# Optimization experiments

Measured on AMD Instinct MI355X. Metric: run time of the kernel, lower is better.

The kernel has to match this reference:

```python
import jax, jax.numpy as jnp
import numpy as np

NEG = -1e30


def setup_inputs() -> dict:
    key = jax.random.key(0)
    ks = jax.random.split(key, 8)
    B, d, Lc, Lq = 32, 128, 2048, 512
    C = jax.random.normal(ks[0], (B, d, Lc), dtype=jnp.float32)
    Q = jax.random.normal(ks[1], (B, d, Lq), dtype=jnp.float32)
    Cmask = jax.random.randint(ks[2], (B, Lc), 0, 2, dtype=jnp.int32)
    Qmask = jax.random.randint(ks[3], (B, Lq), 0, 2, dtype=jnp.int32)
    # xavier_uniform over (d, 1): bound = sqrt(6 / (d + 1))
    bnd = float(np.sqrt(6.0 / (d + 1)))
    w_c = jax.random.uniform(ks[4], (d, 1), minval=-bnd, maxval=bnd, dtype=jnp.float32)
    w_q = jax.random.uniform(ks[5], (d, 1), minval=-bnd, maxval=bnd, dtype=jnp.float32)
    bnd_m = float(np.sqrt(6.0 / (1 + d)))
    w_mul = jax.random.uniform(ks[6], (1, 1, d), minval=-bnd_m, maxval=bnd_m, dtype=jnp.float32)
    bias = jnp.zeros((1,), dtype=jnp.float32)
    return {"C": C, "Q": Q, "Cmask": Cmask, "Qmask": Qmask,
            "w_c": w_c, "w_q": w_q, "w_mul": w_mul, "bias": bias}


def reference(C, Q, Cmask, Qmask, w_c, w_q, w_mul, bias):
    # C: [B, d, Lc], Q: [B, d, Lq] -> transpose to token-major
    Ct = jnp.swapaxes(C, 1, 2)  # [B, Lc, d]
    Qt = jnp.swapaxes(Q, 1, 2)  # [B, Lq, d]
    cm = Cmask.astype(jnp.float32)[:, :, None]   # [B, Lc, 1]
    qm = Qmask.astype(jnp.float32)[:, None, :]   # [B, 1, Lq]
    # optimized trilinear similarity S: [B, Lc, Lq] (dropout p=0 / eval mode)
    s0 = Ct @ w_c                                  # [B, Lc, 1]
    s1 = jnp.swapaxes(Qt @ w_q, 1, 2)              # [B, 1, Lq]
    s2 = jnp.einsum('bcd,bqd->bcq', Ct * w_mul, Qt)  # [B, Lc, Lq]
    S = s0 + s1 + s2 + bias
    S1 = jax.nn.softmax(S + NEG * (1.0 - qm), axis=2)  # mask over query axis
    S2 = jax.nn.softmax(S + NEG * (1.0 - cm), axis=1)  # mask over context axis
    A = jnp.einsum('bcq,bqd->bcd', S1, Qt)             # [B, Lc, d]
    Bm = jnp.einsum('bck,bkd->bcd', jnp.einsum('bcq,bkq->bck', S1, S2), Ct)
    out = jnp.concatenate([Ct, A, Ct * A, Ct * Bm], axis=2)  # [B, Lc, 4d]
    return jnp.swapaxes(out, 1, 2)  # [B, 4d, Lc]
```

## Files before the change

kernel.cpp:

```cpp
#include <hip/hip_runtime.h>

#define B_ 32
#define D_ 128
#define LC 2048
#define LQ 512
#define CCH 16
#define RCH 4

#define NEGINF (-3.0e38f)

typedef __attribute__((ext_vector_type(8))) short bf16x8;
typedef __attribute__((ext_vector_type(4))) float f32x4;
typedef __attribute__((ext_vector_type(8))) unsigned short us8;
typedef __attribute__((ext_vector_type(8))) _Float16 f16x8;

__device__ __forceinline__ unsigned short bf16rne(float x) {
    unsigned int u = __float_as_uint(x);
    u = (u + 0x7FFFu + ((u >> 16) & 1u)) >> 16;
    return (unsigned short)u;
}

__device__ __forceinline__ void gll16(const void* g, void* l) {
    __builtin_amdgcn_global_load_lds((const __attribute__((address_space(1))) void*)g,
                                     (__attribute__((address_space(3))) void*)l, 16, 0, 0);
}

__global__ void k_dotw(const float* __restrict__ X, const float* __restrict__ w,
                       float* __restrict__ outv, int L) {
    int idx = blockIdx.x * 256 + threadIdx.x;
    int b = idx / L, x = idx - b * L;
    const float* Xp = X + (size_t)b * D_ * L + x;
    float acc = 0.f;
#pragma unroll 8
    for (int dd = 0; dd < D_; ++dd) acc += Xp[(size_t)dd * L] * w[dd];
    outv[idx] = acc;
}

__global__ void k_prep_C(const float* __restrict__ C, const float* __restrict__ wmul,
                         short* __restrict__ Ctw, short* __restrict__ Cb16) {
    int b = blockIdx.y, c0 = blockIdx.x * 64;
    __shared__ float Tf[128][65];
    __shared__ float wm[128];
    int t = threadIdx.x;
    if (t < 128) wm[t] = wmul[t];
    const float* Cb = C + (size_t)b * D_ * LC;
#pragma unroll
    for (int i = 0; i < 8; ++i) {
        int idx = t + i * 256;
        int d = idx >> 4, c4 = idx & 15;
        float4 v = *(const float4*)(Cb + (size_t)d * LC + c0 + c4 * 4);
        Tf[d][c4 * 4 + 0] = v.x; Tf[d][c4 * 4 + 1] = v.y;
        Tf[d][c4 * 4 + 2] = v.z; Tf[d][c4 * 4 + 3] = v.w;
        ushort4 cv;
        cv.x = bf16rne(v.x); cv.y = bf16rne(v.y); cv.z = bf16rne(v.z); cv.w = bf16rne(v.w);
        *(ushort4*)(Cb16 + ((size_t)b * D_ + d) * LC + c0 + c4 * 4) = cv;
    }
    __syncthreads();
    int c_l = t & 63, g = t >> 6;
    unsigned short u[32];
#pragma unroll
    for (int j = 0; j < 32; ++j) {
        int d = g * 32 + j;
        u[j] = bf16rne(Tf[d][c_l] * wm[d]);
    }
    short* dst = Ctw + ((size_t)b * LC + c0 + c_l) * D_ + g * 32;
#pragma unroll
    for (int k = 0; k < 4; ++k) *(us8*)(dst + k * 8) = *(const us8*)&u[k * 8];
}

__global__ void k_prep_Q(const float* __restrict__ Q, short* __restrict__ Qt16,
                         short* __restrict__ Wf) {
    int b = blockIdx.y, q0 = blockIdx.x * 64;
    __shared__ float Tf[128][65];
    int t = threadIdx.x;
    const float* Qb = Q + (size_t)b * D_ * LQ;
#pragma unroll
    for (int i = 0; i < 8; ++i) {
        int idx = t + i * 256;
        int d = idx >> 4, q4 = idx & 15;
        float4 v = *(const float4*)(Qb + (size_t)d * LQ + q0 + q4 * 4);
        Tf[d][q4 * 4 + 0] = v.x; Tf[d][q4 * 4 + 1] = v.y;
        Tf[d][q4 * 4 + 2] = v.z; Tf[d][q4 * 4 + 3] = v.w;
        ushort4 cv;
        cv.x = bf16rne(v.x); cv.y = bf16rne(v.y); cv.z = bf16rne(v.z); cv.w = bf16rne(v.w);
        *(ushort4*)(Wf + ((size_t)b * 256 + d) * LQ + q0 + q4 * 4) = cv;
    }
    __syncthreads();
    int q_l = t & 63, g = t >> 6;
    unsigned short u[32];
#pragma unroll
    for (int j = 0; j < 32; ++j) u[j] = bf16rne(Tf[g * 32 + j][q_l]);
    short* dst = Qt16 + ((size_t)b * LQ + q0 + q_l) * D_ + g * 32;
#pragma unroll
    for (int k = 0; k < 4; ++k) *(us8*)(dst + k * 8) = *(const us8*)&u[k * 8];
}

__global__ __launch_bounds__(256) void k_S_mfma(const short* __restrict__ Ctw,
                                                const short* __restrict__ Qt16,
                                                const float* __restrict__ s0,
                                                const float* __restrict__ s1,
                                                const float* __restrict__ bias,
                                                const int* __restrict__ Cmask,
                                                const int* __restrict__ Qmask,
                                                _Float16* __restrict__ S16,
                                                float* __restrict__ pm,
                                                float* __restrict__ pl,
                                                float* __restrict__ plr) {
    int b = blockIdx.y;
    int cT = blockIdx.x >> 2, qT = blockIdx.x & 3;
    int c0 = cT * 128, q0 = qT * 128;
    int t = threadIdx.x, w = t >> 6, l = t & 63;
    int wm_ = w >> 1, wn = w & 1;
    __shared__ short As[128 * 64];
    __shared__ short Bs[128 * 64];
    f32x4 acc[4][4] = {};
    const short* Arow = Ctw + ((size_t)b * LC + c0) * D_;
    const short* Brow = Qt16 + ((size_t)b * LQ + q0) * D_;
    int lr = l >> 3, sl = l & 7;
    for (int kt = 0; kt < 2; ++kt) {
        __syncthreads();
#pragma unroll
        for (int i = 0; i < 4; ++i) {
            int r = w * 32 + i * 8 + lr;
            int g = sl ^ (r & 7);
            gll16(Arow + (size_t)r * D_ + kt * 64 + g * 8, &As[(w * 32 + i * 8) * 64]);
            gll16(Brow + (size_t)r * D_ + kt * 64 + g * 8, &Bs[(w * 32 + i * 8) * 64]);
        }
        __syncthreads();
#pragma unroll
        for (int ks = 0; ks < 2; ++ks) {
            int kg = ks * 4 + (l >> 4);
            bf16x8 af[4], bfr[4];
#pragma unroll
            for (int ms = 0; ms < 4; ++ms) {
                int m = wm_ * 64 + ms * 16 + (l & 15);
                af[ms] = *(const bf16x8*)&As[m * 64 + (kg ^ (m & 7)) * 8];
            }
#pragma unroll
            for (int ns = 0; ns < 4; ++ns) {
                int n = wn * 64 + ns * 16 + (l & 15);
                bfr[ns] = *(const bf16x8*)&Bs[n * 64 + (kg ^ (n & 7)) * 8];
            }
#pragma unroll
            for (int ms = 0; ms < 4; ++ms)
#pragma unroll
                for (int ns = 0; ns < 4; ++ns)
                    acc[ms][ns] = __builtin_amdgcn_mfma_f32_16x16x32_bf16(af[ms], bfr[ns], acc[ms][ns], 0, 0, 0);
        }
    }
    float bv = bias[0];
    float s0v[16];
    int cmv[16];
#pragma unroll
    for (int ms = 0; ms < 4; ++ms) {
        int cb = c0 + wm_ * 64 + ms * 16 + (l >> 4) * 4;
        float4 sv = *(const float4*)(s0 + b * LC + cb);
        s0v[ms * 4 + 0] = sv.x; s0v[ms * 4 + 1] = sv.y;
        s0v[ms * 4 + 2] = sv.z; s0v[ms * 4 + 3] = sv.w;
        int4 cv = *(const int4*)(Cmask + b * LC + cb);
        cmv[ms * 4 + 0] = cv.x; cmv[ms * 4 + 1] = cv.y;
        cmv[ms * 4 + 2] = cv.z; cmv[ms * 4 + 3] = cv.w;
    }
    float rs_[16];
#pragma unroll
    for (int k = 0; k < 16; ++k) rs_[k] = 0.f;
    __syncthreads();
    float* Mp = (float*)As;
    float* Lp = (float*)Bs;
    float* Rsf = (float*)As + 2048;
    int prow = wm_ * 4 + (l >> 4);
#pragma unroll
    for (int ns = 0; ns < 4; ++ns) {
        int qi = wn * 64 + ns * 16 + (l & 15);
        int q = q0 + qi;
        float s1v = s1[b * LQ + q] + bv;
        int qmn = Qmask[b * LQ + q];
        float vq16[16];
#pragma unroll
        for (int ms = 0; ms < 4; ++ms) {
            int cb = c0 + wm_ * 64 + ms * 16 + (l >> 4) * 4;
#pragma unroll
            for (int r = 0; r < 4; ++r) {
                float vf = acc[ms][ns][r] + s0v[ms * 4 + r] + s1v;
                _Float16 h = (_Float16)vf;
                S16[((size_t)b * LC + cb + r) * LQ + q] = h;
                vq16[ms * 4 + r] = (float)h;
            }
        }
        float mt = NEGINF;
#pragma unroll
        for (int k = 0; k < 16; ++k) mt = fmaxf(mt, cmv[k] ? vq16[k] : NEGINF);
        float st = 0.f;
#pragma unroll
        for (int k = 0; k < 16; ++k) st += cmv[k] ? __expf(vq16[k] - mt) : 0.f;
        Mp[prow * 132 + qi] = mt;
        Lp[prow * 132 + qi] = st;
#pragma unroll
        for (int k = 0; k < 16; ++k) rs_[k] += qmn ? __expf(vq16[k]) : 0.f;
    }
#pragma unroll
    for (int off = 1; off < 16; off <<= 1)
#pragma unroll
        for (int k = 0; k < 16; ++k) rs_[k] += __shfl_xor(rs_[k], off, 64);
    if ((l & 15) == 0) {
#pragma unroll
        for (int ms = 0; ms < 4; ++ms)
#pragma unroll
            for (int r = 0; r < 4; ++r) {
                int cl = wm_ * 64 + ms * 16 + (l >> 4) * 4 + r;
                Rsf[wn * 128 + cl] = rs_[ms * 4 + r];
            }
    }
    __syncthreads();
    if (t < 128) {
        float mm = Mp[t], ll = Lp[t];
#pragma unroll
        for (int g = 1; g < 8; ++g) {
            float m2 = Mp[g * 132 + t], l2 = Lp[g * 132 + t];
            float mn = fmaxf(mm, m2);
            ll = ll * __expf(mm - mn) + l2 * __expf(m2 - mn);
            mm = mn;
        }
        size_t o = ((size_t)cT * B_ + b) * LQ + q0 + t;
        pm[o] = mm; pl[o] = ll;
        size_t orow = ((size_t)qT * B_ + b) * LC + c0 + t;
        plr[orow] = Rsf[t] + Rsf[128 + t];
    }
}

__global__ void k_comb(const float* __restrict__ pm, const float* __restrict__ pl,
                       const float* __restrict__ plr,
                       float* __restrict__ colmax, float* __restrict__ colsum,
                       float* __restrict__ rowsum) {
    int bx = blockIdx.x;
    if (bx < (B_ * LQ) / 256) {
        int idx = bx * 256 + threadIdx.x;
        float m = NEGINF, l = 0.f;
#pragma unroll
        for (int ch = 0; ch < CCH; ++ch) {
            float m2 = pm[(size_t)ch * B_ * LQ + idx];
            float l2 = pl[(size_t)ch * B_ * LQ + idx];
            float mn = fmaxf(m, m2);
            l = l * __expf(m - mn) + l2 * __expf(m2 - mn);
            m = mn;
        }
        colmax[idx] = m; colsum[idx] = l;
    } else {
        int idx = (bx - (B_ * LQ) / 256) * 256 + threadIdx.x;
        float s = 0.f;
#pragma unroll
        for (int ch = 0; ch < RCH; ++ch) s += plr[(size_t)ch * B_ * LC + idx];
        rowsum[idx] = s;
    }
}

__global__ __launch_bounds__(256) void k_V2_mfma(const short* __restrict__ Cb16,
                                                 _Float16* __restrict__ S16,
                                                 const int* __restrict__ Cmask,
                                                 const int* __restrict__ Qmask,
                                                 const float* __restrict__ colmax,
                                                 const float* __restrict__ colsum,
                                                 const float* __restrict__ rowsum,
                                                 short* __restrict__ Wf) {
    int b = blockIdx.y;
    int q0 = blockIdx.x * 64;
    int t = threadIdx.x, w = t >> 6, l = t & 63;
    __shared__ short As[128 * 64];
    __shared__ short Bs[64 * 72];
    f32x4 acc[2][4] = {};
    const short* Arow = Cb16 + (size_t)b * D_ * LC;
    int lr = l >> 3, sl = l & 7;
    float cmx[16];
#pragma unroll
    for (int j2 = 0; j2 < 4; ++j2)
        *(float4*)&cmx[j2 * 4] = *(const float4*)(colmax + b * LQ + q0 + w * 16 + j2 * 4);
    int qmv[16];
#pragma unroll
    for (int j2 = 0; j2 < 4; ++j2)
        *(int4*)&qmv[j2 * 4] = *(const int4*)(Qmask + b * LQ + q0 + w * 16 + j2 * 4);
    _Float16* Sq = S16 + (size_t)b * LC * LQ + q0 + w * 16;
    const int* cmb = Cmask + b * LC;
    const float* rsb = rowsum + b * LC;

    for (int kt = 0; kt < 32; ++kt) {
        int ck = kt * 64;
        __builtin_amdgcn_s_barrier();
        __builtin_amdgcn_sched_barrier(0);
#pragma unroll
        for (int i = 0; i < 4; ++i) {
            int r = w * 32 + i * 8 + lr;
            int g = sl ^ (r & 7);
            gll16(Arow + (size_t)r * LC + ck + g * 8, &As[(w * 32 + i * 8) * 64]);
        }
        {
            int c = ck + l;
            float cmf = (float)cmb[c];
            float ri = 1.0f / rsb[c];
            _Float16* sp = Sq + (size_t)c * LQ;
            f16x8 v0 = *(const f16x8*)sp;
            f16x8 v1 = *(const f16x8*)(sp + 8);
#pragma unroll
            for (int j = 0; j < 8; ++j)
                Bs[(w * 16 + j) * 72 + l] = (short)bf16rne(cmf * __expf((float)v0[j] - cmx[j]));
#pragma unroll
            for (int j = 0; j < 8; ++j)
                Bs[(w * 16 + 8 + j) * 72 + l] = (short)bf16rne(cmf * __expf((float)v1[j] - cmx[8 + j]));
            unsigned short p0[8], p1r[8];
#pragma unroll
            for (int j = 0; j < 8; ++j)
                p0[j] = qmv[j] ? bf16rne(__expf((float)v0[j]) * ri) : (unsigned short)0;
#pragma unroll
            for (int j = 0; j < 8; ++j)
                p1r[j] = qmv[8 + j] ? bf16rne(__expf((float)v1[j]) * ri) : (unsigned short)0;
            __builtin_amdgcn_sched_barrier(0);
            *(us8*)sp = *(const us8*)&p0[0];
            *(us8*)(sp + 8) = *(const us8*)&p1r[0];
        }
        asm volatile("s_waitcnt vmcnt(2) lgkmcnt(0)" ::: "memory");
        __builtin_amdgcn_s_barrier();
        __builtin_amdgcn_sched_barrier(0);
#pragma unroll
        for (int ks = 0; ks < 2; ++ks) {
            int kg = ks * 4 + (l >> 4);
            bf16x8 af[2], bfr[4];
#pragma unroll
            for (int ms = 0; ms < 2; ++ms) {
                int m = w * 32 + ms * 16 + (l & 15);
                af[ms] = *(const bf16x8*)&As[m * 64 + (kg ^ (m & 7)) * 8];
            }
#pragma unroll
            for (int ns = 0; ns < 4; ++ns) {
                int n = ns * 16 + (l & 15);
                bfr[ns] = *(const bf16x8*)&Bs[n * 72 + kg * 8];
            }
#pragma unroll
            for (int ms = 0; ms < 2; ++ms)
#pragma unroll
                for (int ns = 0; ns < 4; ++ns)
                    acc[ms][ns] = __builtin_amdgcn_mfma_f32_16x16x32_bf16(af[ms], bfr[ns], acc[ms][ns], 0, 0, 0);
        }
    }
#pragma unroll
    for (int ms = 0; ms < 2; ++ms)
#pragma unroll
        for (int ns = 0; ns < 4; ++ns) {
            int q = q0 + ns * 16 + (l & 15);
            float csi = 1.0f / colsum[b * LQ + q];
#pragma unroll
            for (int r = 0; r < 4; ++r) {
                int dd = w * 32 + ms * 16 + (l >> 4) * 4 + r;
                Wf[((size_t)b * 256 + 128 + dd) * LQ + q] = (short)bf16rne(acc[ms][ns][r] * csi);
            }
        }
}

__global__ __launch_bounds__(512) void k_out_mfma(const short* __restrict__ P1,
                                                  const short* __restrict__ Wf,
                                                  const float* __restrict__ C,
                                                  float* __restrict__ out) {
    int b = blockIdx.y;
    int c0 = blockIdx.x * 128;
    int t = threadIdx.x, w = t >> 6, l = t & 63;
    int wn = w & 3, wc = w >> 2;
    __shared__ short As[2 * 256 * 64];
    __shared__ short Bs[2 * 128 * 64];
    f32x4 acc[4][4] = {};
    const short* Arow = Wf + (size_t)b * 256 * LQ;
    const short* Brow = P1 + ((size_t)b * LC + c0) * LQ;
    int lr = l >> 3, sl = l & 7;
    int g = sl ^ lr;

#define STAGE(p, kt)                                                              \
    {                                                                             \
        short* Ad = As + (p) * (256 * 64);                                        \
        short* Bd = Bs + (p) * (128 * 64);                                        \
        _Pragma("unroll")                                                         \
        for (int i = 0; i < 4; ++i) {                                             \
            int r = w * 32 + i * 8 + lr;                                          \
            gll16(Arow + (size_t)r * LQ + (kt) * 64 + g * 8,                      \
                  &Ad[(w * 32 + i * 8) * 64]);                                    \
        }                                                                         \
        _Pragma("unroll")                                                         \
        for (int i = 0; i < 2; ++i) {                                             \
            int r = w * 16 + i * 8 + lr;                                          \
            gll16(Brow + (size_t)r * LQ + (kt) * 64 + g * 8,                      \
                  &Bd[(w * 16 + i * 8) * 64]);                                    \
        }                                                                         \
    }

    STAGE(0, 0);
    int cur = 0;
    for (int kt = 0; kt < 8; ++kt) {
        if (kt < 7) {
            STAGE(cur ^ 1, kt + 1);
            asm volatile("s_waitcnt vmcnt(6)" ::: "memory");
        } else {
            asm volatile("s_waitcnt vmcnt(0)" ::: "memory");
        }
        __builtin_amdgcn_s_barrier();
        __builtin_amdgcn_sched_barrier(0);
        const short* Ac = As + cur * (256 * 64);
        const short* Bc = Bs + cur * (128 * 64);
#pragma unroll
        for (int ks = 0; ks < 2; ++ks) {
            int kg = ks * 4 + (l >> 4);
            bf16x8 af[4], bfr[4];
#pragma unroll
            for (int ms = 0; ms < 4; ++ms) {
                int m = wn * 64 + ms * 16 + (l & 15);
                af[ms] = *(const bf16x8*)&Ac[m * 64 + (kg ^ (m & 7)) * 8];
            }
#pragma unroll
            for (int ns = 0; ns < 4; ++ns) {
                int cc = wc * 64 + ns * 16 + (l & 15);
                bfr[ns] = *(const bf16x8*)&Bc[cc * 64 + (kg ^ (cc & 7)) * 8];
            }
#pragma unroll
            for (int ms = 0; ms < 4; ++ms)
#pragma unroll
                for (int ns = 0; ns < 4; ++ns)
                    acc[ms][ns] = __builtin_amdgcn_mfma_f32_16x16x32_bf16(af[ms], bfr[ns], acc[ms][ns], 0, 0, 0);
        }
        __builtin_amdgcn_s_barrier();
        cur ^= 1;
    }
#undef STAGE
#pragma unroll
    for (int ms = 0; ms < 4; ++ms) {
        int nb = wn * 64 + ms * 16 + (l >> 4) * 4;
#pragma unroll
        for (int ns = 0; ns < 4; ++ns) {
            int c = c0 + wc * 64 + ns * 16 + (l & 15);
#pragma unroll
            for (int r = 0; r < 4; ++r) {
                int n = nb + r;
                float a = acc[ms][ns][r];
                if (n < 128) {
                    float cv = C[((size_t)b * D_ + n) * LC + c];
                    out[((size_t)b * 512 + n) * LC + c] = cv;
                    out[((size_t)b * 512 + 128 + n) * LC + c] = a;
                    out[((size_t)b * 512 + 256 + n) * LC + c] = cv * a;
                } else {
                    int dd = n - 128;
                    float cv = C[((size_t)b * D_ + dd) * LC + c];
                    out[((size_t)b * 512 + 384 + dd) * LC + c] = cv * a;
                }
            }
        }
    }
}

extern "C" void kernel_launch(void* const* d_in, const int* in_sizes, int n_in,
                              void* d_out, int out_size, void* d_ws, size_t ws_size,
                              hipStream_t stream) {
    const float* C     = (const float*)d_in[0];
    const float* Q     = (const float*)d_in[1];
    const int*   Cmask = (const int*)d_in[2];
    const int*   Qmask = (const int*)d_in[3];
    const float* w_c   = (const float*)d_in[4];
    const float* w_q   = (const float*)d_in[5];
    const float* w_mul = (const float*)d_in[6];
    const float* bias  = (const float*)d_in[7];
    float* out = (float*)d_out;

    _Float16* S16 = (_Float16*)d_ws;
    short* Cb16 = (short*)(S16 + (size_t)B_ * LC * LQ);
    short* Ctw  = Cb16 + (size_t)B_ * D_ * LC;
    short* Qt16 = Ctw + (size_t)B_ * LC * D_;
    short* Wf   = Qt16 + (size_t)B_ * LQ * D_;
    float* s0     = (float*)(Wf + (size_t)B_ * 256 * LQ);
    float* s1     = s0 + B_ * LC;
    float* colmax = s1 + B_ * LQ;
    float* colsum = colmax + B_ * LQ;
    float* rowsum = colsum + B_ * LQ;
    float* pm     = rowsum + B_ * LC;
    float* pl     = pm + (size_t)CCH * B_ * LQ;
    float* plr    = pl + (size_t)CCH * B_ * LQ;

    hipLaunchKernelGGL(k_dotw, dim3(B_ * LC / 256), dim3(256), 0, stream, C, w_c, s0, LC);
    hipLaunchKernelGGL(k_dotw, dim3(B_ * LQ / 256), dim3(256), 0, stream, Q, w_q, s1, LQ);
    hipLaunchKernelGGL(k_prep_C, dim3(LC / 64, B_), dim3(256), 0, stream, C, w_mul, Ctw, Cb16);
    hipLaunchKernelGGL(k_prep_Q, dim3(LQ / 64, B_), dim3(256), 0, stream, Q, Qt16, Wf);
    hipLaunchKernelGGL(k_S_mfma, dim3((LC / 128) * (LQ / 128), B_), dim3(256), 0, stream,
                       Ctw, Qt16, s0, s1, bias, Cmask, Qmask, S16, pm, pl, plr);
    hipLaunchKernelGGL(k_comb, dim3((B_ * LQ + B_ * LC) / 256), dim3(256), 0, stream,
                       pm, pl, plr, colmax, colsum, rowsum);
    hipLaunchKernelGGL(k_V2_mfma, dim3(LQ / 64, B_), dim3(256), 0, stream,
                       Cb16, S16, Cmask, Qmask, colmax, colsum, rowsum, Wf);
    hipLaunchKernelGGL(k_out_mfma, dim3(LC / 128, B_), dim3(512), 0, stream,
                       (const short*)S16, Wf, C, out);
}
```

Baseline: 386.8 us.

## Move row-softmax P1 computation from V2 kernel into output GEMM B-tile load

The V2 kernel no longer rewrites the S16 buffer in place with row-normalized softmax probabilities. Instead, k_out_mfma loads raw fp16 S values into registers, applies exp, row-sum normalization and the query mask, then writes bf16 into LDS. This removes one full write pass over the large B×Lc×Lq buffer and moves exp work into the output GEMM. Loads are now issued two tiles ahead through registers. The trade-off is extra ALU work and register pressure inside the output GEMM loop.

```diff
diff --git a/kernel.cpp b/kernel.cpp
--- a/kernel.cpp
+++ b/kernel.cpp
@@ -255,12 +255,10 @@
 }
 
 __global__ __launch_bounds__(256) void k_V2_mfma(const short* __restrict__ Cb16,
-                                                 _Float16* __restrict__ S16,
+                                                 const _Float16* __restrict__ S16,
                                                  const int* __restrict__ Cmask,
-                                                 const int* __restrict__ Qmask,
                                                  const float* __restrict__ colmax,
                                                  const float* __restrict__ colsum,
-                                                 const float* __restrict__ rowsum,
                                                  short* __restrict__ Wf) {
     int b = blockIdx.y;
     int q0 = blockIdx.x * 64;
@@ -274,13 +272,8 @@
 #pragma unroll
     for (int j2 = 0; j2 < 4; ++j2)
         *(float4*)&cmx[j2 * 4] = *(const float4*)(colmax + b * LQ + q0 + w * 16 + j2 * 4);
-    int qmv[16];
-#pragma unroll
-    for (int j2 = 0; j2 < 4; ++j2)
-        *(int4*)&qmv[j2 * 4] = *(const int4*)(Qmask + b * LQ + q0 + w * 16 + j2 * 4);
-    _Float16* Sq = S16 + (size_t)b * LC * LQ + q0 + w * 16;
+    const _Float16* Sq = S16 + (size_t)b * LC * LQ + q0 + w * 16;
     const int* cmb = Cmask + b * LC;
-    const float* rsb = rowsum + b * LC;
 
     for (int kt = 0; kt < 32; ++kt) {
         int ck = kt * 64;
@@ -295,8 +288,7 @@
         {
             int c = ck + l;
             float cmf = (float)cmb[c];
-            float ri = 1.0f / rsb[c];
-            _Float16* sp = Sq + (size_t)c * LQ;
+            const _Float16* sp = Sq + (size_t)c * LQ;
             f16x8 v0 = *(const f16x8*)sp;
             f16x8 v1 = *(const f16x8*)(sp + 8);
 #pragma unroll
@@ -305,18 +297,8 @@
 #pragma unroll
             for (int j = 0; j < 8; ++j)
                 Bs[(w * 16 + 8 + j) * 72 + l] = (short)bf16rne(cmf * __expf((float)v1[j] - cmx[8 + j]));
-            unsigned short p0[8], p1r[8];
-#pragma unroll
-            for (int j = 0; j < 8; ++j)
-                p0[j] = qmv[j] ? bf16rne(__expf((float)v0[j]) * ri) : (unsigned short)0;
-#pragma unroll
-            for (int j = 0; j < 8; ++j)
-                p1r[j] = qmv[8 + j] ? bf16rne(__expf((float)v1[j]) * ri) : (unsigned short)0;
-            __builtin_amdgcn_sched_barrier(0);
-            *(us8*)sp = *(const us8*)&p0[0];
-            *(us8*)(sp + 8) = *(const us8*)&p1r[0];
-        }
-        asm volatile("s_waitcnt vmcnt(2) lgkmcnt(0)" ::: "memory");
+        }
+        asm volatile("s_waitcnt vmcnt(0) lgkmcnt(0)" ::: "memory");
         __builtin_amdgcn_s_barrier();
         __builtin_amdgcn_sched_barrier(0);
 #pragma unroll
@@ -354,9 +336,11 @@
         }
 }
 
-__global__ __launch_bounds__(512) void k_out_mfma(const short* __restrict__ P1,
+__global__ __launch_bounds__(512) void k_out_mfma(const _Float16* __restrict__ S16,
                                                   const short* __restrict__ Wf,
                                                   const float* __restrict__ C,
+                                                  const int* __restrict__ Qmask,
+                                                  const float* __restrict__ rowsum,
                                                   float* __restrict__ out) {
     int b = blockIdx.y;
     int c0 = blockIdx.x * 128;
@@ -364,39 +348,60 @@
     int wn = w & 3, wc = w >> 2;
     __shared__ short As[2 * 256 * 64];
     __shared__ short Bs[2 * 128 * 64];
+    __shared__ float Qm[LQ];
     f32x4 acc[4][4] = {};
     const short* Arow = Wf + (size_t)b * 256 * LQ;
-    const short* Brow = P1 + ((size_t)b * LC + c0) * LQ;
+    const _Float16* Brow = S16 + ((size_t)b * LC + c0) * LQ;
     int lr = l >> 3, sl = l & 7;
     int g = sl ^ lr;
-
-#define STAGE(p, kt)                                                              \
+    int r0 = w * 16 + lr, r1 = r0 + 8;
+    float ri0 = 1.0f / rowsum[b * LC + c0 + r0];
+    float ri1 = 1.0f / rowsum[b * LC + c0 + r1];
+    Qm[t] = (float)Qmask[b * LQ + t];
+    __syncthreads();
+
+#define STAGE_A(p, kt)                                                            \
     {                                                                             \
         short* Ad = As + (p) * (256 * 64);                                        \
-        short* Bd = Bs + (p) * (128 * 64);                                        \
         _Pragma("unroll")                                                         \
         for (int i = 0; i < 4; ++i) {                                             \
             int r = w * 32 + i * 8 + lr;                                          \
             gll16(Arow + (size_t)r * LQ + (kt) * 64 + g * 8,                      \
                   &Ad[(w * 32 + i * 8) * 64]);                                    \
         }                                                                         \
-        _Pragma("unroll")                                                         \
-        for (int i = 0; i < 2; ++i) {                                             \
-            int r = w * 16 + i * 8 + lr;                                          \
-            gll16(Brow + (size_t)r * LQ + (kt) * 64 + g * 8,                      \
-                  &Bd[(w * 16 + i * 8) * 64]);                                    \
-        }                                                                         \
-    }
-
-    STAGE(0, 0);
+    }
+#define LOAD_B(v0_, v1_, kt)                                                      \
+    v0_ = *(const f16x8*)(Brow + (size_t)r0 * LQ + (kt) * 64 + g * 8);            \
+    v1_ = *(const f16x8*)(Brow + (size_t)r1 * LQ + (kt) * 64 + g * 8);
+
+    f16x8 bA0, bA1, bB0, bB1;
+    LOAD_B(bA0, bA1, 0);
+    STAGE_A(0, 0);
+    LOAD_B(bB0, bB1, 1);
+    STAGE_A(1, 1);
+    __builtin_amdgcn_sched_barrier(0);
     int cur = 0;
     for (int kt = 0; kt < 8; ++kt) {
-        if (kt < 7) {
-            STAGE(cur ^ 1, kt + 1);
-            asm volatile("s_waitcnt vmcnt(6)" ::: "memory");
-        } else {
-            asm volatile("s_waitcnt vmcnt(0)" ::: "memory");
-        }
+        if (kt < 7) asm volatile("s_waitcnt vmcnt(6)" ::: "memory");
+        else        asm volatile("s_waitcnt vmcnt(0)" ::: "memory");
+        {
+            f16x8 v0 = (kt & 1) ? bB0 : bA0;
+            f16x8 v1 = (kt & 1) ? bB1 : bA1;
+            float qm[8];
+#pragma unroll
+            for (int j = 0; j < 8; ++j) qm[j] = Qm[kt * 64 + g * 8 + j];
+            unsigned short p0[8], p1[8];
+#pragma unroll
+            for (int j = 0; j < 8; ++j)
+                p0[j] = (qm[j] != 0.f) ? bf16rne(__expf((float)v0[j]) * ri0) : (unsigned short)0;
+#pragma unroll
+            for (int j = 0; j < 8; ++j)
+                p1[j] = (qm[j] != 0.f) ? bf16rne(__expf((float)v1[j]) * ri1) : (unsigned short)0;
+            short* Bd = Bs + cur * (128 * 64);
+            *(us8*)&Bd[r0 * 64 + sl * 8] = *(const us8*)&p0[0];
+            *(us8*)&Bd[r1 * 64 + sl * 8] = *(const us8*)&p1[0];
+        }
+        asm volatile("s_waitcnt lgkmcnt(0)" ::: "memory");
         __builtin_amdgcn_s_barrier();
         __builtin_amdgcn_sched_barrier(0);
         const short* Ac = As + cur * (256 * 64);
@@ -422,9 +427,16 @@
                     acc[ms][ns] = __builtin_amdgcn_mfma_f32_16x16x32_bf16(af[ms], bfr[ns], acc[ms][ns], 0, 0, 0);
         }
         __builtin_amdgcn_s_barrier();
+        __builtin_amdgcn_sched_barrier(0);
+        if (kt < 6) {
+            if (kt & 1) { LOAD_B(bB0, bB1, kt + 2); }
+            else        { LOAD_B(bA0, bA1, kt + 2); }
+            STAGE_A(cur, kt + 2);
+        }
         cur ^= 1;
     }
-#undef STAGE
+#undef STAGE_A
+#undef LOAD_B
 #pragma unroll
     for (int ms = 0; ms < 4; ++ms) {
         int nb = wn * 64 + ms * 16 + (l >> 4) * 4;
@@ -486,7 +498,7 @@
     hipLaunchKernelGGL(k_comb, dim3((B_ * LQ + B_ * LC) / 256), dim3(256), 0, stream,
                        pm, pl, plr, colmax, colsum, rowsum);
     hipLaunchKernelGGL(k_V2_mfma, dim3(LQ / 64, B_), dim3(256), 0, stream,
-                       Cb16, S16, Cmask, Qmask, colmax, colsum, rowsum, Wf);
+                       Cb16, S16, Cmask, colmax, colsum, Wf);
     hipLaunchKernelGGL(k_out_mfma, dim3(LC / 128, B_), dim3(512), 0, stream,
-                       (const short*)S16, Wf, C, out);
-}
+                       S16, Wf, C, Qmask, rowsum, out);
+}
```

Result: faster. 378.1 us (-2.2%).
